# Kernel optimization log

Hardware: AMD Instinct MI355X
Metric: run time of the kernel (lower is better)

## Reference

```python
import jax, jax.numpy as jnp
import numpy as np
from jax import lax


def setup_inputs() -> dict:
    key = jax.random.key(0)
    k1, k2 = jax.random.split(key)
    B, H, W, C = 8, 32, 32, 512
    N = 16384
    feature_batch = jax.random.normal(k1, (B, H, W, C), dtype=jnp.float32)
    mb = jax.random.normal(k2, (N, C), dtype=jnp.float32)
    return {"feature_batch": feature_batch, "mb": mb, "b": 9}


def reference(feature_batch, mb, b):
    B, H, W, C = feature_batch.shape
    fv = feature_batch.reshape(B * H * W, C)                       # (Q, C)
    sq = (
        jnp.sum(fv * fv, axis=1)[:, None]
        + jnp.sum(mb * mb, axis=1)[None, :]
        - 2.0 * (fv @ mb.T)
    )                                                               # (Q, N)
    sq = jnp.maximum(sq, 0.0)  # guard fp round-off before sqrt
    # smallest-b distances, sorted ascending (top_k of negated values)
    neg_topk = lax.top_k(-sq, b)[0]                                 # (Q, b)
    top_k_dists_squared = -neg_topk
    pixel_scores = jnp.sqrt(top_k_dists_squared[:, 0]).reshape(B, H * W)
    max_idx = jnp.argmax(pixel_scores, axis=1)                      # (B,)
    softmax_args = jnp.sqrt(
        top_k_dists_squared.reshape(B, H * W, b)[jnp.arange(B), max_idx, :]
    )                                                               # (B, b)
    image_scores = softmax_args[:, 0]
    if b > 1:
        image_scores = image_scores * (1.0 - jax.nn.softmax(softmax_args, axis=1)[:, 0])
    pixel_scores = pixel_scores.reshape(B, 1, H, W)
    return pixel_scores, image_scores
```

## Files before the change

kernel.cpp:

```cpp
#include <hip/hip_runtime.h>

typedef unsigned short u16;

#define M_ROWS 8192
#define N_ROWS 16384
#define KDIM   512
#define BM     256
#define BN     128
#define BK     64
#define NCHUNKS 16
#define NPER   (N_ROWS / NCHUNKS)
#define TOPK   9

typedef __attribute__((ext_vector_type(8)))  short bf16x8;
typedef __attribute__((ext_vector_type(16))) float f32x16;

__device__ __forceinline__ void gload_lds16(const void* g, void* l) {
  __builtin_amdgcn_global_load_lds(
      (const __attribute__((address_space(1))) void*)g,
      (__attribute__((address_space(3))) void*)l,
      16, 0, 0);
}

__device__ __forceinline__ u16 f2bf(float x) {
  union { float f; unsigned u; } c; c.f = x;
  unsigned u = c.u;
  u += 0x7fffu + ((u >> 16) & 1u);
  return (u16)(u >> 16);
}

__device__ __forceinline__ void topk_update(float v, float* best) {
  if (v < best[TOPK - 1]) {
    #pragma unroll
    for (int i = 0; i < TOPK; ++i) {
      float b = best[i];
      best[i] = fminf(b, v);
      v = fmaxf(b, v);
    }
  }
}

__global__ __launch_bounds__(256) void prep_kernel(
    const float* __restrict__ fv, const float* __restrict__ mb,
    u16* __restrict__ fvb, u16* __restrict__ mbb,
    float* __restrict__ nf, float* __restrict__ nm_perm)
{
  int idx = blockIdx.x * 4 + (threadIdx.x >> 6);
  int l = threadIdx.x & 63;
  const float* src; u16* dst;
  if (idx < M_ROWS) {
    src = fv + (size_t)idx * KDIM; dst = fvb + (size_t)idx * KDIM;
  } else {
    int r = idx - M_ROWS;
    src = mb + (size_t)r * KDIM; dst = mbb + (size_t)r * KDIM;
  }
  float4 x0 = ((const float4*)src)[2 * l];
  float4 x1 = ((const float4*)src)[2 * l + 1];
  float s = x0.x * x0.x + x0.y * x0.y + x0.z * x0.z + x0.w * x0.w
          + x1.x * x1.x + x1.y * x1.y + x1.z * x1.z + x1.w * x1.w;
  uint4 o;
  o.x = (unsigned)f2bf(x0.x) | ((unsigned)f2bf(x0.y) << 16);
  o.y = (unsigned)f2bf(x0.z) | ((unsigned)f2bf(x0.w) << 16);
  o.z = (unsigned)f2bf(x1.x) | ((unsigned)f2bf(x1.y) << 16);
  o.w = (unsigned)f2bf(x1.z) | ((unsigned)f2bf(x1.w) << 16);
  ((uint4*)dst)[l] = o;
  #pragma unroll
  for (int off = 32; off > 0; off >>= 1) s += __shfl_down(s, off, 64);
  if (l == 0) {
    if (idx < M_ROWS) {
      nf[idx] = s;
    } else {
      int n  = idx - M_ROWS;
      int ig = n >> 5;
      int w5 = n & 31;
      int h  = (w5 >> 2) & 1;
      int r  = (w5 & 3) | ((w5 >> 3) << 2);
      nm_perm[(ig * 2 + h) * 16 + r] = s;
    }
  }
}

__global__ __launch_bounds__(256, 2) void gemm_topk_kernel(
    const u16* __restrict__ fvb, const u16* __restrict__ mbb,
    const float* __restrict__ nm_perm, float* __restrict__ partial)
{
  __shared__ __align__(16) u16 As[BM * BK];
  __shared__ __align__(16) u16 Bs[BN * BK];

  const int t   = threadIdx.x;
  const int l   = t & 63;
  const int w   = t >> 6;
  const int h   = l >> 5;
  const int c31 = l & 31;
  const int cx  = c31 & 7;

  const int m0    = blockIdx.x * BM;
  const int ncoff = blockIdx.y * NPER;

  const int srow_lo = l >> 3;
  const int sc      = ((l & 7) ^ srow_lo) * 8;

  float best[2][TOPK];
  float T[2];
  #pragma unroll
  for (int s = 0; s < 2; ++s) {
    T[s] = 3.4e38f;
    #pragma unroll
    for (int i = 0; i < TOPK; ++i) best[s][i] = 3.4e38f;
  }

  for (int nt = 0; nt < NPER / BN; ++nt) {
    const int nbase = ncoff + nt * BN;
    f32x16 acc[2][4];
    #pragma unroll
    for (int s = 0; s < 2; ++s)
      #pragma unroll
      for (int i = 0; i < 4; ++i)
        #pragma unroll
        for (int r = 0; r < 16; ++r) acc[s][i][r] = 0.0f;

    for (int kc = 0; kc < KDIM / BK; ++kc) {
      __syncthreads();
      const int kb = kc * BK + sc;
      #pragma unroll
      for (int i = 0; i < 8; ++i)
        gload_lds16(fvb + (size_t)(m0 + w * 64 + i * 8 + srow_lo) * KDIM + kb,
                    &As[(w * 64 + i * 8) * BK]);
      #pragma unroll
      for (int i = 0; i < 4; ++i)
        gload_lds16(mbb + (size_t)(nbase + w * 32 + i * 8 + srow_lo) * KDIM + kb,
                    &Bs[(w * 32 + i * 8) * BK]);
      __syncthreads();
      #pragma unroll
      for (int kk = 0; kk < 4; ++kk) {
        const int ch = ((kk * 2 + h) ^ cx) * 8;
        bf16x8 f0 = *(const bf16x8*)&As[(w * 64 +      c31) * BK + ch];
        bf16x8 f1 = *(const bf16x8*)&As[(w * 64 + 32 + c31) * BK + ch];
        #pragma unroll
        for (int i = 0; i < 4; ++i) {
          bf16x8 mbf = *(const bf16x8*)&Bs[(i * 32 + c31) * BK + ch];
          acc[0][i] = __builtin_amdgcn_mfma_f32_32x32x16_bf16(mbf, f0, acc[0][i], 0, 0, 0);
          acc[1][i] = __builtin_amdgcn_mfma_f32_32x32x16_bf16(mbf, f1, acc[1][i], 0, 0, 0);
        }
      }
    }

    #pragma unroll
    for (int i = 0; i < 4; ++i) {
      const float4* np = (const float4*)&nm_perm[(((nbase >> 5) + i) * 2 + h) * 16];
      float4 q0 = np[0], q1 = np[1], q2 = np[2], q3 = np[3];
      #pragma unroll
      for (int s = 0; s < 2; ++s) {
        float v[16];
        v[ 0] = fmaf(-2.0f, acc[s][i][ 0], q0.x);
        v[ 1] = fmaf(-2.0f, acc[s][i][ 1], q0.y);
        v[ 2] = fmaf(-2.0f, acc[s][i][ 2], q0.z);
        v[ 3] = fmaf(-2.0f, acc[s][i][ 3], q0.w);
        v[ 4] = fmaf(-2.0f, acc[s][i][ 4], q1.x);
        v[ 5] = fmaf(-2.0f, acc[s][i][ 5], q1.y);
        v[ 6] = fmaf(-2.0f, acc[s][i][ 6], q1.z);
        v[ 7] = fmaf(-2.0f, acc[s][i][ 7], q1.w);
        v[ 8] = fmaf(-2.0f, acc[s][i][ 8], q2.x);
        v[ 9] = fmaf(-2.0f, acc[s][i][ 9], q2.y);
        v[10] = fmaf(-2.0f, acc[s][i][10], q2.z);
        v[11] = fmaf(-2.0f, acc[s][i][11], q2.w);
        v[12] = fmaf(-2.0f, acc[s][i][12], q3.x);
        v[13] = fmaf(-2.0f, acc[s][i][13], q3.y);
        v[14] = fmaf(-2.0f, acc[s][i][14], q3.z);
        v[15] = fmaf(-2.0f, acc[s][i][15], q3.w);
        float bmin = 3.4e38f;
        #pragma unroll
        for (int r = 0; r < 16; ++r) bmin = fminf(bmin, v[r]);
        if (bmin < T[s]) {
          #pragma unroll
          for (int r = 0; r < 16; ++r) topk_update(v[r], best[s]);
          T[s] = best[s][TOPK - 1];
        }
      }
    }
    #pragma unroll
    for (int s = 0; s < 2; ++s)
      T[s] = fminf(best[s][TOPK - 1], __shfl_xor(best[s][TOPK - 1], 32, 64));
  }

  #pragma unroll
  for (int s = 0; s < 2; ++s) {
    float tmp[TOPK];
    #pragma unroll
    for (int q = 0; q < TOPK; ++q) tmp[q] = __shfl_xor(best[s][q], 32, 64);
    #pragma unroll
    for (int q = 0; q < TOPK; ++q) topk_update(tmp[q], best[s]);
    int m = m0 + w * 64 + s * 32 + c31;
    size_t base = ((size_t)blockIdx.y * M_ROWS + m) * TOPK;
    if (h == 0) {
      #pragma unroll
      for (int q = 0; q < 5; ++q) partial[base + q] = best[s][q];
    } else {
      #pragma unroll
      for (int q = 5; q < TOPK; ++q) partial[base + q] = best[s][q];
    }
  }
}

__global__ __launch_bounds__(256) void merge_kernel(
    const float* __restrict__ partial, const float* __restrict__ nf,
    float* __restrict__ final9, float* __restrict__ out_pix)
{
  int row = blockIdx.x * 256 + threadIdx.x;
  float best[TOPK];
  #pragma unroll
  for (int i = 0; i < TOPK; ++i) best[i] = 3.4e38f;
  for (int s = 0; s < NCHUNKS; ++s) {
    const float* p = &partial[((size_t)s * M_ROWS + row) * TOPK];
    #pragma unroll
    for (int i = 0; i < TOPK; ++i) topk_update(p[i], best);
  }
  float nfr = nf[row];
  float d[TOPK];
  #pragma unroll
  for (int i = 0; i < TOPK; ++i) d[i] = sqrtf(fmaxf(best[i] + nfr, 0.0f));
  out_pix[row] = d[0];
  #pragma unroll
  for (int i = 0; i < TOPK; ++i) final9[(size_t)row * TOPK + i] = d[i];
}

__global__ __launch_bounds__(256) void img_kernel(
    const float* __restrict__ out_pix, const float* __restrict__ final9,
    const int* __restrict__ bptr, float* __restrict__ out_img)
{
  int img = blockIdx.x, t = threadIdx.x;
  float bv = -1.0f; int bi = 0;
  for (int p = t; p < 1024; p += 256) {
    float v = out_pix[img * 1024 + p];
    if (v > bv) { bv = v; bi = p; }
  }
  __shared__ float sv[256];
  __shared__ int   si[256];
  sv[t] = bv; si[t] = bi;
  __syncthreads();
  for (int off = 128; off > 0; off >>= 1) {
    if (t < off) {
      float v2 = sv[t + off]; int i2 = si[t + off];
      if (v2 > sv[t] || (v2 == sv[t] && i2 < si[t])) { sv[t] = v2; si[t] = i2; }
    }
    __syncthreads();
  }
  if (t == 0) {
    int row = img * 1024 + si[0];
    int b = bptr[0];
    float s0 = final9[(size_t)row * TOPK + 0];
    float score = s0;
    if (b > 1) {
      int bb = b < TOPK ? b : TOPK;
      float mx = s0;
      for (int i = 1; i < bb; ++i) mx = fmaxf(mx, final9[(size_t)row * TOPK + i]);
      float den = 0.0f;
      for (int i = 0; i < bb; ++i) den += expf(final9[(size_t)row * TOPK + i] - mx);
      score = s0 * (1.0f - expf(s0 - mx) / den);
    }
    out_img[img] = score;
  }
}

extern "C" void kernel_launch(void* const* d_in, const int* in_sizes, int n_in,
                              void* d_out, int out_size, void* d_ws, size_t ws_size,
                              hipStream_t stream) {
  const float* fv   = (const float*)d_in[0];
  const float* mb   = (const float*)d_in[1];
  const int*   bptr = (const int*)d_in[2];
  float* out = (float*)d_out;

  char* ws = (char*)d_ws;
  u16*   fvb     = (u16*)ws;
  u16*   mbb     = (u16*)(ws + 8388608);
  float* nf      = (float*)(ws + 25165824);
  float* nm_perm = (float*)(ws + 25198592);
  float* partial = (float*)(ws + 25264128);
  float* final9  = (float*)(ws + 29982720);

  hipLaunchKernelGGL(prep_kernel, dim3((M_ROWS + N_ROWS) / 4), dim3(256), 0, stream,
                     fv, mb, fvb, mbb, nf, nm_perm);
  hipLaunchKernelGGL(gemm_topk_kernel, dim3(M_ROWS / BM, NCHUNKS), dim3(256), 0, stream,
                     fvb, mbb, nm_perm, partial);
  hipLaunchKernelGGL(merge_kernel, dim3(M_ROWS / 256), dim3(256), 0, stream,
                     partial, nf, final9, out);
  hipLaunchKernelGGL(img_kernel, dim3(8), dim3(256), 0, stream,
                     out, final9, bptr, out + M_ROWS);
}
```

Before: 310.1 us.

## Triple-buffer LDS tiles with async global-to-LDS prefetch across flattened GEMM loop

Replaces the single-buffered load-sync-compute loop with a three-stage LDS ring buffer. Tiles are prefetched two steps ahead using direct global-to-LDS loads, with vmcnt waits and a single barrier per step. The n-tile and k-chunk loops are flattened so prefetching carries across n-tile boundaries, BK is halved to 32, and the LDS swizzle is adjusted to match. The goal is to hide global memory latency behind MFMA work. The cost is 72KB of dynamic LDS per block, which may limit occupancy to two blocks per CU, plus twice as many loop iterations.

```diff
diff --git a/kernel.cpp b/kernel.cpp
--- a/kernel.cpp
+++ b/kernel.cpp
@@ -7,10 +7,14 @@
 #define KDIM   512
 #define BM     256
 #define BN     128
-#define BK     64
+#define BK     32
 #define NCHUNKS 16
 #define NPER   (N_ROWS / NCHUNKS)
 #define TOPK   9
+
+#define ASZ (BM * BK)
+#define BSZ (BN * BK)
+#define NTT ((NPER / BN) * (KDIM / BK))
 
 typedef __attribute__((ext_vector_type(8)))  short bf16x8;
 typedef __attribute__((ext_vector_type(16))) float f32x16;
@@ -84,21 +88,42 @@
     const u16* __restrict__ fvb, const u16* __restrict__ mbb,
     const float* __restrict__ nm_perm, float* __restrict__ partial)
 {
-  __shared__ __align__(16) u16 As[BM * BK];
-  __shared__ __align__(16) u16 Bs[BN * BK];
+  extern __shared__ __align__(16) u16 sm[];
+  u16* const Asm = sm;
+  u16* const Bsm = sm + 3 * ASZ;
 
   const int t   = threadIdx.x;
   const int l   = t & 63;
   const int w   = t >> 6;
   const int h   = l >> 5;
   const int c31 = l & 31;
-  const int cx  = c31 & 7;
+  const int xr  = (c31 >> 1) & 3;
 
   const int m0    = blockIdx.x * BM;
   const int ncoff = blockIdx.y * NPER;
 
-  const int srow_lo = l >> 3;
-  const int sc      = ((l & 7) ^ srow_lo) * 8;
+  const int srow = l >> 2;
+  const int sc   = ((l & 3) ^ ((l >> 3) & 3)) * 8;
+
+  const u16* aSrc = fvb + (size_t)(m0 + w * 64 + srow) * KDIM + sc;
+  const u16* bSrc = mbb + (size_t)(ncoff + w * 32 + srow) * KDIM + sc;
+
+  const int aRd  = (w * 64 + c31) * BK;
+  const int ch0  = (h ^ xr) * 8;
+  const int ch1  = ch0 ^ 16;
+
+#define STAGE(kc2_, bufS_) do {                                               \
+    const size_t ao_ = (size_t)((kc2_) & 15) * BK;                            \
+    const size_t so_ = (size_t)((kc2_) >> 4) * ((size_t)BN * KDIM) + ao_;     \
+    u16* ad_ = Asm + (bufS_) * ASZ + (w * 64) * BK;                           \
+    u16* bd_ = Bsm + (bufS_) * BSZ + (w * 32) * BK;                           \
+    gload_lds16(aSrc + ao_,                 ad_);                             \
+    gload_lds16(aSrc + ao_ + 16 * KDIM,     ad_ + 16 * BK);                   \
+    gload_lds16(aSrc + ao_ + 32 * KDIM,     ad_ + 32 * BK);                   \
+    gload_lds16(aSrc + ao_ + 48 * KDIM,     ad_ + 48 * BK);                   \
+    gload_lds16(bSrc + so_,                 bd_);                             \
+    gload_lds16(bSrc + so_ + 16 * KDIM,     bd_ + 16 * BK);                   \
+  } while (0)
 
   float best[2][TOPK];
   float T[2];
@@ -109,78 +134,101 @@
     for (int i = 0; i < TOPK; ++i) best[s][i] = 3.4e38f;
   }
 
-  for (int nt = 0; nt < NPER / BN; ++nt) {
-    const int nbase = ncoff + nt * BN;
-    f32x16 acc[2][4];
-    #pragma unroll
-    for (int s = 0; s < 2; ++s)
-      #pragma unroll
-      for (int i = 0; i < 4; ++i)
+  f32x16 acc[2][4];
+
+  STAGE(0, 0);
+  STAGE(1, 1);
+  asm volatile("s_waitcnt vmcnt(6)" ::: "memory");
+  __builtin_amdgcn_s_barrier();
+
+  int bC = 0, bS = 2;
+  for (int tt = 0; tt < NTT; ++tt) {
+    if ((tt & 15) == 0) {
+      #pragma unroll
+      for (int s = 0; s < 2; ++s)
         #pragma unroll
-        for (int r = 0; r < 16; ++r) acc[s][i][r] = 0.0f;
-
-    for (int kc = 0; kc < KDIM / BK; ++kc) {
-      __syncthreads();
-      const int kb = kc * BK + sc;
-      #pragma unroll
-      for (int i = 0; i < 8; ++i)
-        gload_lds16(fvb + (size_t)(m0 + w * 64 + i * 8 + srow_lo) * KDIM + kb,
-                    &As[(w * 64 + i * 8) * BK]);
-      #pragma unroll
-      for (int i = 0; i < 4; ++i)
-        gload_lds16(mbb + (size_t)(nbase + w * 32 + i * 8 + srow_lo) * KDIM + kb,
-                    &Bs[(w * 32 + i * 8) * BK]);
-      __syncthreads();
-      #pragma unroll
-      for (int kk = 0; kk < 4; ++kk) {
-        const int ch = ((kk * 2 + h) ^ cx) * 8;
-        bf16x8 f0 = *(const bf16x8*)&As[(w * 64 +      c31) * BK + ch];
-        bf16x8 f1 = *(const bf16x8*)&As[(w * 64 + 32 + c31) * BK + ch];
+        for (int i = 0; i < 4; ++i)
+          #pragma unroll
+          for (int r = 0; r < 16; ++r) acc[s][i][r] = 0.0f;
+    }
+
+    const int kc2 = tt + 2;
+    if (kc2 < NTT) STAGE(kc2, bS);
+
+    {
+      const u16* Ak = Asm + bC * ASZ;
+      const u16* Bk = Bsm + bC * BSZ;
+      {
+        bf16x8 f0 = *(const bf16x8*)&Ak[aRd + ch0];
+        bf16x8 f1 = *(const bf16x8*)&Ak[aRd + 32 * BK + ch0];
         #pragma unroll
         for (int i = 0; i < 4; ++i) {
-          bf16x8 mbf = *(const bf16x8*)&Bs[(i * 32 + c31) * BK + ch];
+          bf16x8 mbf = *(const bf16x8*)&Bk[(i * 32 + c31) * BK + ch0];
           acc[0][i] = __builtin_amdgcn_mfma_f32_32x32x16_bf16(mbf, f0, acc[0][i], 0, 0, 0);
           acc[1][i] = __builtin_amdgcn_mfma_f32_32x32x16_bf16(mbf, f1, acc[1][i], 0, 0, 0);
         }
       }
-    }
-
-    #pragma unroll
-    for (int i = 0; i < 4; ++i) {
-      const float4* np = (const float4*)&nm_perm[(((nbase >> 5) + i) * 2 + h) * 16];
-      float4 q0 = np[0], q1 = np[1], q2 = np[2], q3 = np[3];
-      #pragma unroll
-      for (int s = 0; s < 2; ++s) {
-        float v[16];
-        v[ 0] = fmaf(-2.0f, acc[s][i][ 0], q0.x);
-        v[ 1] = fmaf(-2.0f, acc[s][i][ 1], q0.y);
-        v[ 2] = fmaf(-2.0f, acc[s][i][ 2], q0.z);
-        v[ 3] = fmaf(-2.0f, acc[s][i][ 3], q0.w);
-        v[ 4] = fmaf(-2.0f, acc[s][i][ 4], q1.x);
-        v[ 5] = fmaf(-2.0f, acc[s][i][ 5], q1.y);
-        v[ 6] = fmaf(-2.0f, acc[s][i][ 6], q1.z);
-        v[ 7] = fmaf(-2.0f, acc[s][i][ 7], q1.w);
-        v[ 8] = fmaf(-2.0f, acc[s][i][ 8], q2.x);
-        v[ 9] = fmaf(-2.0f, acc[s][i][ 9], q2.y);
-        v[10] = fmaf(-2.0f, acc[s][i][10], q2.z);
-        v[11] = fmaf(-2.0f, acc[s][i][11], q2.w);
-        v[12] = fmaf(-2.0f, acc[s][i][12], q3.x);
-        v[13] = fmaf(-2.0f, acc[s][i][13], q3.y);
-        v[14] = fmaf(-2.0f, acc[s][i][14], q3.z);
-        v[15] = fmaf(-2.0f, acc[s][i][15], q3.w);
-        float bmin = 3.4e38f;
+      {
+        bf16x8 f0 = *(const bf16x8*)&Ak[aRd + ch1];
+        bf16x8 f1 = *(const bf16x8*)&Ak[aRd + 32 * BK + ch1];
         #pragma unroll
-        for (int r = 0; r < 16; ++r) bmin = fminf(bmin, v[r]);
-        if (bmin < T[s]) {
-          #pragma unroll
-          for (int r = 0; r < 16; ++r) topk_update(v[r], best[s]);
-          T[s] = best[s][TOPK - 1];
+        for (int i = 0; i < 4; ++i) {
+          bf16x8 mbf = *(const bf16x8*)&Bk[(i * 32 + c31) * BK + ch1];
+          acc[0][i] = __builtin_amdgcn_mfma_f32_32x32x16_bf16(mbf, f0, acc[0][i], 0, 0, 0);
+          acc[1][i] = __builtin_amdgcn_mfma_f32_32x32x16_bf16(mbf, f1, acc[1][i], 0, 0, 0);
         }
       }
     }
-    #pragma unroll
-    for (int s = 0; s < 2; ++s)
-      T[s] = fminf(best[s][TOPK - 1], __shfl_xor(best[s][TOPK - 1], 32, 64));
+
+    if (tt < NTT - 1) {
+      if (tt < NTT - 2) { asm volatile("s_waitcnt vmcnt(6)" ::: "memory"); }
+      else              { asm volatile("s_waitcnt vmcnt(0)" ::: "memory"); }
+      __builtin_amdgcn_s_barrier();
+    }
+
+    if ((tt & 15) == 15) {
+      const int nt    = tt >> 4;
+      const int nbase = ncoff + nt * BN;
+      #pragma unroll
+      for (int i = 0; i < 4; ++i) {
+        const float4* np = (const float4*)&nm_perm[(((nbase >> 5) + i) * 2 + h) * 16];
+        float4 q0 = np[0], q1 = np[1], q2 = np[2], q3 = np[3];
+        #pragma unroll
+        for (int s = 0; s < 2; ++s) {
+          float v[16];
+          v[ 0] = fmaf(-2.0f, acc[s][i][ 0], q0.x);
+          v[ 1] = fmaf(-2.0f, acc[s][i][ 1], q0.y);
+          v[ 2] = fmaf(-2.0f, acc[s][i][ 2], q0.z);
+          v[ 3] = fmaf(-2.0f, acc[s][i][ 3], q0.w);
+          v[ 4] = fmaf(-2.0f, acc[s][i][ 4], q1.x);
+          v[ 5] = fmaf(-2.0f, acc[s][i][ 5], q1.y);
+          v[ 6] = fmaf(-2.0f, acc[s][i][ 6], q1.z);
+          v[ 7] = fmaf(-2.0f, acc[s][i][ 7], q1.w);
+          v[ 8] = fmaf(-2.0f, acc[s][i][ 8], q2.x);
+          v[ 9] = fmaf(-2.0f, acc[s][i][ 9], q2.y);
+          v[10] = fmaf(-2.0f, acc[s][i][10], q2.z);
+          v[11] = fmaf(-2.0f, acc[s][i][11], q2.w);
+          v[12] = fmaf(-2.0f, acc[s][i][12], q3.x);
+          v[13] = fmaf(-2.0f, acc[s][i][13], q3.y);
+          v[14] = fmaf(-2.0f, acc[s][i][14], q3.z);
+          v[15] = fmaf(-2.0f, acc[s][i][15], q3.w);
+          float bmin = 3.4e38f;
+          #pragma unroll
+          for (int r = 0; r < 16; ++r) bmin = fminf(bmin, v[r]);
+          if (bmin < T[s]) {
+            #pragma unroll
+            for (int r = 0; r < 16; ++r) topk_update(v[r], best[s]);
+            T[s] = best[s][TOPK - 1];
+          }
+        }
+      }
+      #pragma unroll
+      for (int s = 0; s < 2; ++s)
+        T[s] = fminf(best[s][TOPK - 1], __shfl_xor(best[s][TOPK - 1], 32, 64));
+    }
+
+    bC = (bC == 2) ? 0 : bC + 1;
+    bS = (bS == 2) ? 0 : bS + 1;
   }
 
   #pragma unroll
@@ -280,8 +328,8 @@
 
   hipLaunchKernelGGL(prep_kernel, dim3((M_ROWS + N_ROWS) / 4), dim3(256), 0, stream,
                      fv, mb, fvb, mbb, nf, nm_perm);
-  hipLaunchKernelGGL(gemm_topk_kernel, dim3(M_ROWS / BM, NCHUNKS), dim3(256), 0, stream,
-                     fvb, mbb, nm_perm, partial);
+  hipLaunchKernelGGL(gemm_topk_kernel, dim3(M_ROWS / BM, NCHUNKS), dim3(256),
+                     73728, stream, fvb, mbb, nm_perm, partial);
   hipLaunchKernelGGL(merge_kernel, dim3(M_ROWS / 256), dim3(256), 0, stream,
                      partial, nf, final9, out);
   hipLaunchKernelGGL(img_kernel, dim3(8), dim3(256), 0, stream,
```

Measured after the change: 312.6 us. Within noise of the previous version (+0.8%).
